# Optimization experiments

Measured on AMD Instinct MI355X. Metric: run time of the kernel, lower is better.

The kernel has to match this reference:

```python
import jax, jax.numpy as jnp
import numpy as np

LAMBDA_ENERGY = 0.1   # CONFIG['lambda_energy']
EPS = 1e-6            # CONFIG['eps']
TEMP = 1.0


def setup_inputs() -> dict:
    key = jax.random.key(0)
    k0, k1, k2, k3, k4 = jax.random.split(key, 5)
    B, S, D, N = 8, 4096, 512, 1024
    z_real = jax.random.normal(k0, (B, S, D), dtype=jnp.float32)
    z_imag = jax.random.normal(k1, (B, S, D), dtype=jnp.float32)
    # prev symbol distribution: a proper simplex distribution over symbols
    prev_sym_dist = jax.nn.softmax(jax.random.normal(k2, (B, S, N), dtype=jnp.float32), axis=-1)
    codebook = jax.random.normal(k3, (N, 2 * D), dtype=jnp.float32) * 0.2
    adjacency_energy = jax.random.normal(k4, (N, N), dtype=jnp.float32)
    return {"z_real": z_real, "z_imag": z_imag, "prev_sym_dist": prev_sym_dist,
            "codebook": codebook, "adjacency_energy": adjacency_energy}


def reference(z_real, z_imag, prev_sym_dist, codebook, adjacency_energy):
    D = z_real.shape[-1]
    z_flat = jnp.concatenate([z_real, z_imag], axis=-1)  # [B,S,2D]

    # squared-distance to codebook entries, normalized by feature dim
    d_content = (jnp.sum(z_flat * z_flat, axis=-1, keepdims=True)
                 + jnp.sum(codebook * codebook, axis=-1)
                 - 2.0 * jnp.einsum('bsd,nd->bsn', z_flat, codebook)) / z_flat.shape[-1]

    # ComplexityModulator (eval mode): running_var buffer == 1.0
    mag = jnp.sqrt(z_real * z_real + z_imag * z_imag)  # |z|
    batch_var = jnp.var(mag, ddof=1)                   # torch .var() is unbiased
    modulation = jax.nn.softplus(batch_var / (1.0 + EPS))

    # graph-bias gating
    graph_bias = jnp.einsum('bsn,nm->bsm', prev_sym_dist, adjacency_energy)
    d_total = d_content - (LAMBDA_ENERGY * modulation) * jax.nn.sigmoid(graph_bias)

    # eval path: soft_one_hot = softmax(logits / temp)
    probs = jax.nn.softmax(-d_total / TEMP, axis=-1)   # [B,S,N]
    z_q_flat = jnp.einsum('bsn,nd->bsd', probs, codebook)  # [B,S,2D]

    energy = jnp.mean(d_total)
    return z_q_flat[..., :D], z_q_flat[..., D:], energy
```

## Files before the change

kernel.cpp:

```cpp
#include <hip/hip_runtime.h>

typedef float    floatx4 __attribute__((ext_vector_type(4)));
typedef short    short8  __attribute__((ext_vector_type(8)));
typedef _Float16 h4      __attribute__((ext_vector_type(4)));

#define NROWS 32768
#define KD    1024
#define DD    512

__device__ __forceinline__ unsigned pk_bf16(unsigned hi_bits, unsigned lo_bits) {
    return __builtin_amdgcn_perm(hi_bits, lo_bits, 0x07060302u);
}

__device__ __forceinline__ void gload_lds16(const void* g, void* l) {
    __builtin_amdgcn_global_load_lds((__attribute__((address_space(1))) void*)(void*)g,
                                     (__attribute__((address_space(3))) void*)l,
                                     16, 0, 0);
}

__global__ void k_row(const float* __restrict__ zr, const float* __restrict__ zi,
                      unsigned short* __restrict__ zb,
                      float* __restrict__ zz, float* __restrict__ mgp) {
    int r = blockIdx.x, t = threadIdx.x;
    const float2* a2 = (const float2*)(zr + (size_t)r * DD);
    const float2* b2 = (const float2*)(zi + (size_t)r * DD);
    float2 a = a2[t], b = b2[t];
    unsigned* zrow = (unsigned*)(zb + (size_t)r * KD);
    zrow[t]       = pk_bf16(__float_as_uint(a.y), __float_as_uint(a.x));
    zrow[256 + t] = pk_bf16(__float_as_uint(b.y), __float_as_uint(b.x));
    float m0 = a.x * a.x + b.x * b.x;
    float m1 = a.y * a.y + b.y * b.y;
    float sm2 = m0 + m1;
    float smg = sqrtf(m0) + sqrtf(m1);
    for (int o = 32; o > 0; o >>= 1) { sm2 += __shfl_down(sm2, o); smg += __shfl_down(smg, o); }
    __shared__ float r2[4], rg[4];
    int wv = t >> 6, ln = t & 63;
    if (ln == 0) { r2[wv] = sm2; rg[wv] = smg; }
    __syncthreads();
    if (t == 0) {
        zz[r]  = r2[0] + r2[1] + r2[2] + r2[3];
        mgp[r] = rg[0] + rg[1] + rg[2] + rg[3];
    }
}

__global__ void k_prev(const float* __restrict__ p, unsigned short* __restrict__ pb) {
    size_t i = ((size_t)blockIdx.x * 256 + threadIdx.x) * 8;
    const uint4* g = (const uint4*)(p + i);
    uint4 u0 = g[0], u1 = g[1];
    uint4 o;
    o.x = pk_bf16(u0.y, u0.x); o.y = pk_bf16(u0.w, u0.z);
    o.z = pk_bf16(u1.y, u1.x); o.w = pk_bf16(u1.w, u1.z);
    *(uint4*)(pb + i) = o;
}

__global__ void k_cb(const float* __restrict__ cb, unsigned short* __restrict__ cb_bf,
                     float* __restrict__ cc) {
    int n = blockIdx.x, t = threadIdx.x;
    const float4* src = (const float4*)(cb + (size_t)n * KD);
    float4 v = src[t];
    float s = v.x * v.x + v.y * v.y + v.z * v.z + v.w * v.w;
    unsigned d0 = pk_bf16(__float_as_uint(v.y), __float_as_uint(v.x));
    unsigned d1 = pk_bf16(__float_as_uint(v.w), __float_as_uint(v.z));
    *(uint2*)(cb_bf + (size_t)n * KD + t * 4) = make_uint2(d0, d1);
    for (int o = 32; o > 0; o >>= 1) s += __shfl_down(s, o);
    __shared__ float rd[4];
    int wv = t >> 6, ln = t & 63;
    if (ln == 0) rd[wv] = s;
    __syncthreads();
    if (t == 0) cc[n] = rd[0] + rd[1] + rd[2] + rd[3];
}

__global__ void k_tr(const float* __restrict__ src, unsigned short* __restrict__ dst) {
    __shared__ float tile[32][33];
    int bx = blockIdx.x * 32, by = blockIdx.y * 32;
    int tx = threadIdx.x, ty = threadIdx.y;
    for (int r = ty; r < 32; r += 8)
        tile[r][tx] = src[(size_t)(by + r) * 1024 + bx + tx];
    __syncthreads();
    for (int r = ty; r < 32; r += 8)
        dst[(size_t)(bx + r) * 1024 + by + tx] =
            (unsigned short)(__float_as_uint(tile[tx][r]) >> 16);
}

__global__ void k_scalar(const float* __restrict__ zz, const float* __restrict__ mgp,
                         double* __restrict__ sums, float* __restrict__ lam) {
    int t = threadIdx.x;
    double s2 = 0.0, sg = 0.0;
    for (int i = t; i < NROWS; i += 1024) { s2 += (double)zz[i]; sg += (double)mgp[i]; }
    __shared__ double l2[1024], lg[1024];
    l2[t] = s2; lg[t] = sg; __syncthreads();
    for (int s = 512; s > 0; s >>= 1) {
        if (t < s) { l2[t] += l2[t + s]; lg[t] += lg[t + s]; }
        __syncthreads();
    }
    if (t == 0) {
        double M = 16777216.0;
        double var = (l2[0] - lg[0] * lg[0] / M) / (M - 1.0);
        double x = var / (1.0 + 1e-6);
        double mod = log1p(exp(x));
        lam[0] = (float)(0.1 * mod);
        sums[1] = l2[0];
    }
}

__global__ __launch_bounds__(512, 4)
void k_gemm12(const unsigned short* __restrict__ zb,
              const unsigned short* __restrict__ pb,
              const unsigned short* __restrict__ cb_bf,
              const unsigned short* __restrict__ adjT_bf,
              const float* __restrict__ cc, const float* __restrict__ lam_p,
              _Float16* __restrict__ s_out, double* __restrict__ e_acc) {
    __shared__ unsigned short A1[128 * 64], A2[128 * 64], B1[128 * 64], B2[128 * 64];
    int tid = threadIdx.x, bid = blockIdx.x;
    int wg = (bid & 7) * 256 + (bid >> 3);
    int rt = wg >> 3, ct = wg & 7;
    int row0 = rt * 128, col0 = ct * 128;
    int wv = tid >> 6, ln = tid & 63;
    int wr = (wv >> 1) * 32;
    int wc = (wv & 1) * 64;

    floatx4 acc1[2][4], acc2[2][4];
    for (int i = 0; i < 2; ++i)
        for (int j = 0; j < 4; ++j) {
            floatx4 z4 = {0.f, 0.f, 0.f, 0.f};
            acc1[i][j] = z4; acc2[i][j] = z4;
        }

    int r0 = tid >> 3,         s0 = tid & 7;
    int r1 = (512 + tid) >> 3;
    size_t aoff0 = (size_t)(row0 + r0) * KD + ((s0 ^ (r0 & 7)) << 3);
    size_t aoff1 = (size_t)(row0 + r1) * KD + ((s0 ^ (r1 & 7)) << 3);
    size_t boff0 = (size_t)(col0 + r0) * KD + ((s0 ^ (r0 & 7)) << 3);
    size_t boff1 = (size_t)(col0 + r1) * KD + ((s0 ^ (r1 & 7)) << 3);
    int l0 = wv * 512;
    int l1 = 4096 + wv * 512;

    for (int kb = 0; kb < KD; kb += 64) {
        gload_lds16(zb      + aoff0 + kb, &A1[l0]);
        gload_lds16(zb      + aoff1 + kb, &A1[l1]);
        gload_lds16(pb      + aoff0 + kb, &A2[l0]);
        gload_lds16(pb      + aoff1 + kb, &A2[l1]);
        gload_lds16(cb_bf   + boff0 + kb, &B1[l0]);
        gload_lds16(cb_bf   + boff1 + kb, &B1[l1]);
        gload_lds16(adjT_bf + boff0 + kb, &B2[l0]);
        gload_lds16(adjT_bf + boff1 + kb, &B2[l1]);
        __syncthreads();

        #pragma unroll
        for (int kk = 0; kk < 2; ++kk) {
            int sb = kk * 4 + (ln >> 4);
            short8 af[2], bfr[4];
            #pragma unroll
            for (int i = 0; i < 2; ++i) {
                int r = wr + i * 16 + (ln & 15);
                af[i] = *(const short8*)&A1[r * 64 + ((sb ^ (r & 7)) << 3)];
            }
            #pragma unroll
            for (int j = 0; j < 4; ++j) {
                int r = wc + j * 16 + (ln & 15);
                bfr[j] = *(const short8*)&B1[r * 64 + ((sb ^ (r & 7)) << 3)];
            }
            #pragma unroll
            for (int mi = 0; mi < 2; ++mi)
                #pragma unroll
                for (int ni = 0; ni < 4; ++ni)
                    acc1[mi][ni] = __builtin_amdgcn_mfma_f32_16x16x32_bf16(af[mi], bfr[ni], acc1[mi][ni], 0, 0, 0);
            #pragma unroll
            for (int i = 0; i < 2; ++i) {
                int r = wr + i * 16 + (ln & 15);
                af[i] = *(const short8*)&A2[r * 64 + ((sb ^ (r & 7)) << 3)];
            }
            #pragma unroll
            for (int j = 0; j < 4; ++j) {
                int r = wc + j * 16 + (ln & 15);
                bfr[j] = *(const short8*)&B2[r * 64 + ((sb ^ (r & 7)) << 3)];
            }
            #pragma unroll
            for (int mi = 0; mi < 2; ++mi)
                #pragma unroll
                for (int ni = 0; ni < 4; ++ni)
                    acc2[mi][ni] = __builtin_amdgcn_mfma_f32_16x16x32_bf16(af[mi], bfr[ni], acc2[mi][ni], 0, 0, 0);
        }
        __syncthreads();
    }

    float lam = *lam_p;
    float esum = 0.f;
    for (int mi = 0; mi < 2; ++mi) {
        int rbase = row0 + wr + mi * 16 + (ln >> 4) * 4;
        for (int ni = 0; ni < 4; ++ni) {
            int col = col0 + wc + ni * 16 + (ln & 15);
            float ccol = cc[col];
            for (int r2 = 0; r2 < 4; ++r2) {
                float d1 = acc1[mi][ni][r2];
                float d2 = acc2[mi][ni][r2];
                float sv = (ccol - 2.f * d1) * (1.0f / 1024.0f) - lam / (1.f + __expf(-d2));
                esum += sv;
                s_out[(size_t)(rbase + r2) * KD + col] = (_Float16)sv;
            }
        }
    }
    for (int o = 32; o > 0; o >>= 1) esum += __shfl_down(esum, o);
    if (ln == 0) atomicAdd(e_acc, (double)esum);
}

__global__ void k_softmax(_Float16* __restrict__ sp) {
    int row = blockIdx.x, t = threadIdx.x;
    int wv = t >> 6, ln = t & 63;
    _Float16* srow = sp + (size_t)row * KD;
    h4 v = *(const h4*)(srow + t * 4);
    float x0 = -(float)v.x, x1 = -(float)v.y, x2 = -(float)v.z, x3 = -(float)v.w;
    float mx = fmaxf(fmaxf(x0, x1), fmaxf(x2, x3));
    for (int o = 1; o < 64; o <<= 1) mx = fmaxf(mx, __shfl_xor(mx, o));
    __shared__ float redm[4];
    if (ln == 0) redm[wv] = mx;
    __syncthreads();
    mx = fmaxf(fmaxf(redm[0], redm[1]), fmaxf(redm[2], redm[3]));
    float e0 = __expf(x0 - mx), e1 = __expf(x1 - mx), e2 = __expf(x2 - mx), e3 = __expf(x3 - mx);
    float ss = e0 + e1 + e2 + e3;
    for (int o = 1; o < 64; o <<= 1) ss += __shfl_xor(ss, o);
    __shared__ float reds[4];
    if (ln == 0) reds[wv] = ss;
    __syncthreads();
    ss = reds[0] + reds[1] + reds[2] + reds[3];
    float inv = 1.f / ss;
    unsigned p0 = __float_as_uint(e0 * inv), p1 = __float_as_uint(e1 * inv);
    unsigned p2 = __float_as_uint(e2 * inv), p3 = __float_as_uint(e3 * inv);
    *(uint2*)((unsigned short*)srow + t * 4) = make_uint2(pk_bf16(p1, p0), pk_bf16(p3, p2));
}

__global__ __launch_bounds__(512, 4)
void k_gemm3(const unsigned short* __restrict__ probs,
             const unsigned short* __restrict__ cbT_bf,
             float* __restrict__ outR, float* __restrict__ outI) {
    __shared__ unsigned short At[128 * 64], Bt[128 * 64];
    int tid = threadIdx.x, bid = blockIdx.x;
    int wg = (bid & 7) * 256 + (bid >> 3);
    int rt = wg >> 3, ct = wg & 7;
    int row0 = rt * 128, col0 = ct * 128;
    int wv = tid >> 6, ln = tid & 63;
    int wr = (wv >> 1) * 32;
    int wc = (wv & 1) * 64;

    floatx4 acc[2][4];
    for (int i = 0; i < 2; ++i)
        for (int j = 0; j < 4; ++j) { floatx4 z4 = {0.f, 0.f, 0.f, 0.f}; acc[i][j] = z4; }

    int r0 = tid >> 3,         s0 = tid & 7;
    int r1 = (512 + tid) >> 3;
    size_t aoff0 = (size_t)(row0 + r0) * KD + ((s0 ^ (r0 & 7)) << 3);
    size_t aoff1 = (size_t)(row0 + r1) * KD + ((s0 ^ (r1 & 7)) << 3);
    size_t boff0 = (size_t)(col0 + r0) * KD + ((s0 ^ (r0 & 7)) << 3);
    size_t boff1 = (size_t)(col0 + r1) * KD + ((s0 ^ (r1 & 7)) << 3);
    int l0 = wv * 512;
    int l1 = 4096 + wv * 512;

    for (int kb = 0; kb < KD; kb += 64) {
        gload_lds16(probs  + aoff0 + kb, &At[l0]);
        gload_lds16(probs  + aoff1 + kb, &At[l1]);
        gload_lds16(cbT_bf + boff0 + kb, &Bt[l0]);
        gload_lds16(cbT_bf + boff1 + kb, &Bt[l1]);
        __syncthreads();

        #pragma unroll
        for (int kk = 0; kk < 2; ++kk) {
            int sb = kk * 4 + (ln >> 4);
            short8 af[2], bfr[4];
            #pragma unroll
            for (int i = 0; i < 2; ++i) {
                int r = wr + i * 16 + (ln & 15);
                af[i] = *(const short8*)&At[r * 64 + ((sb ^ (r & 7)) << 3)];
            }
            #pragma unroll
            for (int j = 0; j < 4; ++j) {
                int r = wc + j * 16 + (ln & 15);
                bfr[j] = *(const short8*)&Bt[r * 64 + ((sb ^ (r & 7)) << 3)];
            }
            #pragma unroll
            for (int mi = 0; mi < 2; ++mi)
                #pragma unroll
                for (int ni = 0; ni < 4; ++ni)
                    acc[mi][ni] = __builtin_amdgcn_mfma_f32_16x16x32_bf16(af[mi], bfr[ni], acc[mi][ni], 0, 0, 0);
        }
        __syncthreads();
    }

    for (int mi = 0; mi < 2; ++mi) {
        int rbase = row0 + wr + mi * 16 + (ln >> 4) * 4;
        for (int ni = 0; ni < 4; ++ni) {
            int col = col0 + wc + ni * 16 + (ln & 15);
            for (int r2 = 0; r2 < 4; ++r2) {
                float v = acc[mi][ni][r2];
                size_t row = (size_t)(rbase + r2);
                if (col < DD) outR[row * DD + col] = v;
                else          outI[row * DD + (col - DD)] = v;
            }
        }
    }
}

__global__ void k_final(const double* __restrict__ sums, float* __restrict__ outE) {
    outE[0] = (float)((sums[0] + sums[1]) / 33554432.0);
}

extern "C" void kernel_launch(void* const* d_in, const int* in_sizes, int n_in,
                              void* d_out, int out_size, void* d_ws, size_t ws_size,
                              hipStream_t stream) {
    const float* zr   = (const float*)d_in[0];
    const float* zi   = (const float*)d_in[1];
    const float* prev = (const float*)d_in[2];
    const float* cb   = (const float*)d_in[3];
    const float* adj  = (const float*)d_in[4];
    float* out  = (float*)d_out;
    float* outR = out;
    float* outI = out + (size_t)16777216;
    float* outE = out + (size_t)33554432;

    unsigned short* zb = (unsigned short*)d_out;
    unsigned short* pb = (unsigned short*)d_out + (size_t)33554432;

    char* ws = (char*)d_ws;
    double* sums          = (double*)ws;
    float*  lam           = (float*)(ws + 16);
    float*  zz            = (float*)(ws + 256);
    float*  mgp           = (float*)(ws + 131328);
    float*  cc            = (float*)(ws + 262400);
    unsigned short* cb_bf = (unsigned short*)(ws + 266496);
    unsigned short* adjT  = (unsigned short*)(ws + 2363648);
    unsigned short* cbT   = (unsigned short*)(ws + 4460800);
    _Float16*       sbuf  = (_Float16*)(ws + 6557952);

    hipMemsetAsync(d_ws, 0, 32, stream);
    k_row<<<32768, 256, 0, stream>>>(zr, zi, zb, zz, mgp);
    k_prev<<<16384, 256, 0, stream>>>(prev, pb);
    k_cb<<<1024, 256, 0, stream>>>(cb, cb_bf, cc);
    k_tr<<<dim3(32, 32), dim3(32, 8), 0, stream>>>(adj, adjT);
    k_tr<<<dim3(32, 32), dim3(32, 8), 0, stream>>>(cb, cbT);
    k_scalar<<<1, 1024, 0, stream>>>(zz, mgp, sums, lam);
    k_gemm12<<<2048, 512, 0, stream>>>(zb, pb, cb_bf, adjT, cc, lam, sbuf, sums);
    k_softmax<<<32768, 256, 0, stream>>>(sbuf);
    k_gemm3<<<2048, 512, 0, stream>>>((const unsigned short*)sbuf, cbT, outR, outI);
    k_final<<<1, 1, 0, stream>>>(sums, outE);
}
```

Measured before the change: 698.4 us.

## Split fused dual GEMM and use 4-wave 64x64 per-wave tiles

Splits the fused content and graph-bias GEMM kernel into two separate kernels that share a single main loop. The second kernel reads the fp16 partial scores back and adds the sigmoid term in place. All GEMMs move from 8 waves with 32x64 per-wave tiles to 4 waves with 64x64 per-wave tiles, so each LDS fragment load feeds more MFMAs and LDS use per block is halved in the GEMM12 path. The price is an extra round trip of the 64MB fp16 score buffer, extra rounding of the intermediate to fp16, and higher register pressure from 16 accumulators per wave.

```diff
diff --git a/kernel.cpp b/kernel.cpp
--- a/kernel.cpp
+++ b/kernel.cpp
@@ -103,100 +103,113 @@
     }
 }
 
-__global__ __launch_bounds__(512, 4)
-void k_gemm12(const unsigned short* __restrict__ zb,
-              const unsigned short* __restrict__ pb,
-              const unsigned short* __restrict__ cb_bf,
-              const unsigned short* __restrict__ adjT_bf,
-              const float* __restrict__ cc, const float* __restrict__ lam_p,
-              _Float16* __restrict__ s_out, double* __restrict__ e_acc) {
-    __shared__ unsigned short A1[128 * 64], A2[128 * 64], B1[128 * 64], B2[128 * 64];
+__device__ __forceinline__ void gemm_mainloop(
+    const unsigned short* __restrict__ Ap, const unsigned short* __restrict__ Bp,
+    int row0, int col0, int wv, int ln,
+    unsigned short* As, unsigned short* Bs, floatx4 (&acc)[4][4]) {
+    int wr = (wv >> 1) * 64, wc = (wv & 1) * 64;
+    size_t sa[4], sbo[4];
+    int dst[4];
+    #pragma unroll
+    for (int j = 0; j < 4; ++j) {
+        int g = j * 256 + wv * 64 + ln;
+        int r = g >> 3, s0 = g & 7;
+        size_t co = (size_t)((s0 ^ (r & 7)) << 3);
+        sa[j]  = (size_t)(row0 + r) * KD + co;
+        sbo[j] = (size_t)(col0 + r) * KD + co;
+        dst[j] = (j * 256 + wv * 64) * 8;
+    }
+    for (int kb = 0; kb < KD; kb += 64) {
+        #pragma unroll
+        for (int j = 0; j < 4; ++j) gload_lds16(Ap + sa[j] + kb, &As[dst[j]]);
+        #pragma unroll
+        for (int j = 0; j < 4; ++j) gload_lds16(Bp + sbo[j] + kb, &Bs[dst[j]]);
+        __syncthreads();
+        #pragma unroll
+        for (int kk = 0; kk < 2; ++kk) {
+            int sbi = kk * 4 + (ln >> 4);
+            short8 af[4], bf[4];
+            #pragma unroll
+            for (int i = 0; i < 4; ++i) {
+                int r = wr + i * 16 + (ln & 15);
+                af[i] = *(const short8*)&As[r * 64 + ((sbi ^ (r & 7)) << 3)];
+            }
+            #pragma unroll
+            for (int j = 0; j < 4; ++j) {
+                int r = wc + j * 16 + (ln & 15);
+                bf[j] = *(const short8*)&Bs[r * 64 + ((sbi ^ (r & 7)) << 3)];
+            }
+            #pragma unroll
+            for (int mi = 0; mi < 4; ++mi)
+                #pragma unroll
+                for (int ni = 0; ni < 4; ++ni)
+                    acc[mi][ni] = __builtin_amdgcn_mfma_f32_16x16x32_bf16(af[mi], bf[ni], acc[mi][ni], 0, 0, 0);
+        }
+        __syncthreads();
+    }
+}
+
+__global__ __launch_bounds__(256, 4)
+void k_gemm1(const unsigned short* __restrict__ zb,
+             const unsigned short* __restrict__ cb_bf,
+             const float* __restrict__ cc, _Float16* __restrict__ s_out) {
+    __shared__ unsigned short As[128 * 64], Bs[128 * 64];
     int tid = threadIdx.x, bid = blockIdx.x;
     int wg = (bid & 7) * 256 + (bid >> 3);
     int rt = wg >> 3, ct = wg & 7;
     int row0 = rt * 128, col0 = ct * 128;
     int wv = tid >> 6, ln = tid & 63;
-    int wr = (wv >> 1) * 32;
-    int wc = (wv & 1) * 64;
-
-    floatx4 acc1[2][4], acc2[2][4];
-    for (int i = 0; i < 2; ++i)
-        for (int j = 0; j < 4; ++j) {
-            floatx4 z4 = {0.f, 0.f, 0.f, 0.f};
-            acc1[i][j] = z4; acc2[i][j] = z4;
-        }
-
-    int r0 = tid >> 3,         s0 = tid & 7;
-    int r1 = (512 + tid) >> 3;
-    size_t aoff0 = (size_t)(row0 + r0) * KD + ((s0 ^ (r0 & 7)) << 3);
-    size_t aoff1 = (size_t)(row0 + r1) * KD + ((s0 ^ (r1 & 7)) << 3);
-    size_t boff0 = (size_t)(col0 + r0) * KD + ((s0 ^ (r0 & 7)) << 3);
-    size_t boff1 = (size_t)(col0 + r1) * KD + ((s0 ^ (r1 & 7)) << 3);
-    int l0 = wv * 512;
-    int l1 = 4096 + wv * 512;
-
-    for (int kb = 0; kb < KD; kb += 64) {
-        gload_lds16(zb      + aoff0 + kb, &A1[l0]);
-        gload_lds16(zb      + aoff1 + kb, &A1[l1]);
-        gload_lds16(pb      + aoff0 + kb, &A2[l0]);
-        gload_lds16(pb      + aoff1 + kb, &A2[l1]);
-        gload_lds16(cb_bf   + boff0 + kb, &B1[l0]);
-        gload_lds16(cb_bf   + boff1 + kb, &B1[l1]);
-        gload_lds16(adjT_bf + boff0 + kb, &B2[l0]);
-        gload_lds16(adjT_bf + boff1 + kb, &B2[l1]);
-        __syncthreads();
-
-        #pragma unroll
-        for (int kk = 0; kk < 2; ++kk) {
-            int sb = kk * 4 + (ln >> 4);
-            short8 af[2], bfr[4];
-            #pragma unroll
-            for (int i = 0; i < 2; ++i) {
-                int r = wr + i * 16 + (ln & 15);
-                af[i] = *(const short8*)&A1[r * 64 + ((sb ^ (r & 7)) << 3)];
-            }
-            #pragma unroll
-            for (int j = 0; j < 4; ++j) {
-                int r = wc + j * 16 + (ln & 15);
-                bfr[j] = *(const short8*)&B1[r * 64 + ((sb ^ (r & 7)) << 3)];
-            }
-            #pragma unroll
-            for (int mi = 0; mi < 2; ++mi)
-                #pragma unroll
-                for (int ni = 0; ni < 4; ++ni)
-                    acc1[mi][ni] = __builtin_amdgcn_mfma_f32_16x16x32_bf16(af[mi], bfr[ni], acc1[mi][ni], 0, 0, 0);
-            #pragma unroll
-            for (int i = 0; i < 2; ++i) {
-                int r = wr + i * 16 + (ln & 15);
-                af[i] = *(const short8*)&A2[r * 64 + ((sb ^ (r & 7)) << 3)];
-            }
-            #pragma unroll
-            for (int j = 0; j < 4; ++j) {
-                int r = wc + j * 16 + (ln & 15);
-                bfr[j] = *(const short8*)&B2[r * 64 + ((sb ^ (r & 7)) << 3)];
-            }
-            #pragma unroll
-            for (int mi = 0; mi < 2; ++mi)
-                #pragma unroll
-                for (int ni = 0; ni < 4; ++ni)
-                    acc2[mi][ni] = __builtin_amdgcn_mfma_f32_16x16x32_bf16(af[mi], bfr[ni], acc2[mi][ni], 0, 0, 0);
-        }
-        __syncthreads();
-    }
-
-    float lam = *lam_p;
-    float esum = 0.f;
-    for (int mi = 0; mi < 2; ++mi) {
+    floatx4 acc[4][4];
+    #pragma unroll
+    for (int i = 0; i < 4; ++i)
+        #pragma unroll
+        for (int j = 0; j < 4; ++j) { floatx4 z4 = {0.f, 0.f, 0.f, 0.f}; acc[i][j] = z4; }
+    gemm_mainloop(zb, cb_bf, row0, col0, wv, ln, As, Bs, acc);
+
+    int wr = (wv >> 1) * 64, wc = (wv & 1) * 64;
+    for (int mi = 0; mi < 4; ++mi) {
         int rbase = row0 + wr + mi * 16 + (ln >> 4) * 4;
         for (int ni = 0; ni < 4; ++ni) {
             int col = col0 + wc + ni * 16 + (ln & 15);
             float ccol = cc[col];
             for (int r2 = 0; r2 < 4; ++r2) {
-                float d1 = acc1[mi][ni][r2];
-                float d2 = acc2[mi][ni][r2];
-                float sv = (ccol - 2.f * d1) * (1.0f / 1024.0f) - lam / (1.f + __expf(-d2));
+                float sv = (ccol - 2.f * acc[mi][ni][r2]) * (1.0f / 1024.0f);
+                s_out[(size_t)(rbase + r2) * KD + col] = (_Float16)sv;
+            }
+        }
+    }
+}
+
+__global__ __launch_bounds__(256, 4)
+void k_gemm2(const unsigned short* __restrict__ pb,
+             const unsigned short* __restrict__ adjT_bf,
+             const float* __restrict__ lam_p,
+             _Float16* __restrict__ s_io, double* __restrict__ e_acc) {
+    __shared__ unsigned short As[128 * 64], Bs[128 * 64];
+    int tid = threadIdx.x, bid = blockIdx.x;
+    int wg = (bid & 7) * 256 + (bid >> 3);
+    int rt = wg >> 3, ct = wg & 7;
+    int row0 = rt * 128, col0 = ct * 128;
+    int wv = tid >> 6, ln = tid & 63;
+    floatx4 acc[4][4];
+    #pragma unroll
+    for (int i = 0; i < 4; ++i)
+        #pragma unroll
+        for (int j = 0; j < 4; ++j) { floatx4 z4 = {0.f, 0.f, 0.f, 0.f}; acc[i][j] = z4; }
+    gemm_mainloop(pb, adjT_bf, row0, col0, wv, ln, As, Bs, acc);
+
+    int wr = (wv >> 1) * 64, wc = (wv & 1) * 64;
+    float lam = *lam_p;
+    float esum = 0.f;
+    for (int mi = 0; mi < 4; ++mi) {
+        int rbase = row0 + wr + mi * 16 + (ln >> 4) * 4;
+        for (int ni = 0; ni < 4; ++ni) {
+            int col = col0 + wc + ni * 16 + (ln & 15);
+            for (int r2 = 0; r2 < 4; ++r2) {
+                size_t idx = (size_t)(rbase + r2) * KD + col;
+                float sv = (float)s_io[idx] - lam / (1.f + __expf(-acc[mi][ni][r2]));
                 esum += sv;
-                s_out[(size_t)(rbase + r2) * KD + col] = (_Float16)sv;
+                s_io[idx] = (_Float16)sv;
             }
         }
     }
@@ -229,63 +242,25 @@
     *(uint2*)((unsigned short*)srow + t * 4) = make_uint2(pk_bf16(p1, p0), pk_bf16(p3, p2));
 }
 
-__global__ __launch_bounds__(512, 4)
+__global__ __launch_bounds__(256, 4)
 void k_gemm3(const unsigned short* __restrict__ probs,
              const unsigned short* __restrict__ cbT_bf,
              float* __restrict__ outR, float* __restrict__ outI) {
-    __shared__ unsigned short At[128 * 64], Bt[128 * 64];
+    __shared__ unsigned short As[128 * 64], Bs[128 * 64];
     int tid = threadIdx.x, bid = blockIdx.x;
     int wg = (bid & 7) * 256 + (bid >> 3);
     int rt = wg >> 3, ct = wg & 7;
     int row0 = rt * 128, col0 = ct * 128;
     int wv = tid >> 6, ln = tid & 63;
-    int wr = (wv >> 1) * 32;
-    int wc = (wv & 1) * 64;
-
-    floatx4 acc[2][4];
-    for (int i = 0; i < 2; ++i)
+    floatx4 acc[4][4];
+    #pragma unroll
+    for (int i = 0; i < 4; ++i)
+        #pragma unroll
         for (int j = 0; j < 4; ++j) { floatx4 z4 = {0.f, 0.f, 0.f, 0.f}; acc[i][j] = z4; }
-
-    int r0 = tid >> 3,         s0 = tid & 7;
-    int r1 = (512 + tid) >> 3;
-    size_t aoff0 = (size_t)(row0 + r0) * KD + ((s0 ^ (r0 & 7)) << 3);
-    size_t aoff1 = (size_t)(row0 + r1) * KD + ((s0 ^ (r1 & 7)) << 3);
-    size_t boff0 = (size_t)(col0 + r0) * KD + ((s0 ^ (r0 & 7)) << 3);
-    size_t boff1 = (size_t)(col0 + r1) * KD + ((s0 ^ (r1 & 7)) << 3);
-    int l0 = wv * 512;
-    int l1 = 4096 + wv * 512;
-
-    for (int kb = 0; kb < KD; kb += 64) {
-        gload_lds16(probs  + aoff0 + kb, &At[l0]);
-        gload_lds16(probs  + aoff1 + kb, &At[l1]);
-        gload_lds16(cbT_bf + boff0 + kb, &Bt[l0]);
-        gload_lds16(cbT_bf + boff1 + kb, &Bt[l1]);
-        __syncthreads();
-
-        #pragma unroll
-        for (int kk = 0; kk < 2; ++kk) {
-            int sb = kk * 4 + (ln >> 4);
-            short8 af[2], bfr[4];
-            #pragma unroll
-            for (int i = 0; i < 2; ++i) {
-                int r = wr + i * 16 + (ln & 15);
-                af[i] = *(const short8*)&At[r * 64 + ((sb ^ (r & 7)) << 3)];
-            }
-            #pragma unroll
-            for (int j = 0; j < 4; ++j) {
-                int r = wc + j * 16 + (ln & 15);
-                bfr[j] = *(const short8*)&Bt[r * 64 + ((sb ^ (r & 7)) << 3)];
-            }
-            #pragma unroll
-            for (int mi = 0; mi < 2; ++mi)
-                #pragma unroll
-                for (int ni = 0; ni < 4; ++ni)
-                    acc[mi][ni] = __builtin_amdgcn_mfma_f32_16x16x32_bf16(af[mi], bfr[ni], acc[mi][ni], 0, 0, 0);
-        }
-        __syncthreads();
-    }
-
-    for (int mi = 0; mi < 2; ++mi) {
+    gemm_mainloop(probs, cbT_bf, row0, col0, wv, ln, As, Bs, acc);
+
+    int wr = (wv >> 1) * 64, wc = (wv & 1) * 64;
+    for (int mi = 0; mi < 4; ++mi) {
         int rbase = row0 + wr + mi * 16 + (ln >> 4) * 4;
         for (int ni = 0; ni < 4; ++ni) {
             int col = col0 + wc + ni * 16 + (ln & 15);
@@ -337,8 +312,9 @@
     k_tr<<<dim3(32, 32), dim3(32, 8), 0, stream>>>(adj, adjT);
     k_tr<<<dim3(32, 32), dim3(32, 8), 0, stream>>>(cb, cbT);
     k_scalar<<<1, 1024, 0, stream>>>(zz, mgp, sums, lam);
-    k_gemm12<<<2048, 512, 0, stream>>>(zb, pb, cb_bf, adjT, cc, lam, sbuf, sums);
+    k_gemm1<<<2048, 256, 0, stream>>>(zb, cb_bf, cc, sbuf);
+    k_gemm2<<<2048, 256, 0, stream>>>(pb, adjT, lam, sbuf, sums);
     k_softmax<<<32768, 256, 0, stream>>>(sbuf);
-    k_gemm3<<<2048, 512, 0, stream>>>((const unsigned short*)sbuf, cbT, outR, outI);
+    k_gemm3<<<2048, 256, 0, stream>>>((const unsigned short*)sbuf, cbT, outR, outI);
     k_final<<<1, 1, 0, stream>>>(sums, outE);
 }
```

Result: faster. 646.1 us (-7.5%).
